# Optimization experiments

Hardware: AMD Instinct MI355X
Metric: run time of the kernel (lower is better)

Reference implementation:

```python
import jax, jax.numpy as jnp
import numpy as np

B, S, H, G, W_LOC = 2, 4096, 12, 64, 513  # Longformer-base: window=2*256+1, 64 global slots


def setup_inputs() -> dict:
    key = jax.random.key(0)
    k1, = jax.random.split(key, 1)
    attention_probs = jax.random.uniform(k1, (B, S, H, G + W_LOC), dtype=jnp.float32)
    attention_mask = jnp.zeros((B, S), dtype=jnp.float32)  # all tokens currently kept
    # global tokens are the first G positions of every batch; nonzero(as_tuple) index arrays
    b_idx = jnp.repeat(jnp.arange(B, dtype=jnp.int64), G)
    g_idx = jnp.tile(jnp.arange(G, dtype=jnp.int64), B)
    return {
        "attention_mask": attention_mask,
        "attention_probs": attention_probs,
        "keep_threshold": jnp.asarray(0.005, dtype=jnp.float32),  # base 0.01*6/12 + learned 0
        "max_num_global_attn_indices": G,
        "loc_b": b_idx, "loc_i": g_idx,
        "glob_b": b_idx, "glob_i": g_idx,
    }


def reference(attention_mask, attention_probs, keep_threshold,
              max_num_global_attn_indices, loc_b, loc_i, glob_b, glob_i):
    Gn = max_num_global_attn_indices
    b, s, h, wg = attention_probs.shape
    w = wg - Gn  # local window size, odd
    half = w // 2

    # zero out rows of already-masked tokens (attention_mask < 0)
    probs = jnp.where((attention_mask < 0)[:, :, None, None], 0.0, attention_probs)

    gl = probs[..., :Gn]                              # [B,S,H,G]
    lo = jnp.transpose(probs[..., Gn:], (0, 2, 1, 3))  # [B,H,S,W]

    # anti-diagonal (key-column) sums of the local band; equals the source's
    # conv2d-with-flipped-identity + slice: out[j] = sum_c lo[j + half - c, c]
    lo_p = jnp.pad(lo, ((0, 0), (0, 0), (half, half), (0, 0)))  # [B,H,S+W-1,W]
    rows = jnp.arange(s)[:, None] + (w - 1) - jnp.arange(w)[None, :]  # [S,W]
    diag = lo_p[:, :, rows, jnp.arange(w)[None, :]]  # [B,H,S,W]
    local_sum = diag.sum(axis=(1, 3))                # [B,S] (summed over heads too)

    global_sum = gl.sum(axis=(1, 2))                 # [B,G]
    probs_sum = local_sum.at[loc_b, loc_i].add(global_sum[glob_b, glob_i])

    probs_max = probs_sum.max(axis=-1, keepdims=True)
    scores = probs_sum / probs_max

    thr = jnp.maximum(jnp.float32(1e-5), jnp.asarray(keep_threshold, jnp.float32).reshape(()))
    new_attention_mask = jnp.where(scores < thr, jnp.float32(-10000.0), jnp.float32(0.0))
    return new_attention_mask, scores
```

## Files before the change

### kernel.cpp

```cpp
#include <hip/hip_runtime.h>
#include <float.h>

#define Bsz 2
#define Ssz 4096
#define Hsz 12
#define Gsz 64
#define Wsz 513
#define Csz (Gsz + Wsz)
#define ROW (Hsz * Csz)
#define HALF 256
#define RPB 16
#define WIN (RPB + Wsz - 1)

#define PSUM_SZ ((size_t)Bsz * Ssz)
#define GACC_SZ ((size_t)Bsz * Gsz)

__global__ __launch_bounds__(256) void k1_fused(
    const float* __restrict__ probs, const float* __restrict__ mask,
    float* __restrict__ psum, float* __restrict__ gacc)
{
    __shared__ float win[WIN];
    const int t = threadIdx.x;
    const int row0 = blockIdx.x * RPB;
    const int b = row0 / Ssz;
    float g = 0.f;

    for (int w = t; w < WIN; w += 256) win[w] = 0.f;
    __syncthreads();

    for (int r = 0; r < RPB; ++r) {
        const int row = row0 + r;
        const float* base = probs + (size_t)row * ROW;
        const float scale = (mask[row] < 0.f) ? 0.f : 1.f;

        float v0 = 0.f, v1 = 0.f, v2 = 0.f;
        #pragma unroll
        for (int h = 0; h < Hsz; ++h) {
            const float* hp = base + h * Csz;
            v0 += hp[t];
            v1 += hp[t + 256];
            if (t < Csz - 512)
                v2 += hp[t + 512];
        }
        v0 *= scale; v1 *= scale; v2 *= scale;

        if (t < Gsz) g += v0;
        else atomicAdd(&win[(t - Gsz) + r], v0);
        atomicAdd(&win[(t + 256 - Gsz) + r], v1);
        if (t < Csz - 512)
            atomicAdd(&win[(t + 512 - Gsz) + r], v2);
    }
    __syncthreads();

    const int i_base = (row0 - b * Ssz) - HALF;
    for (int w = t; w < WIN; w += 256) {
        const int i = i_base + w;
        if (i >= 0 && i < Ssz) atomicAdd(&psum[b * Ssz + i], win[w]);
    }
    if (t < Gsz) atomicAdd(&gacc[b * Gsz + t], g);
}

__global__ __launch_bounds__(1024) void k4_final(
    const float* __restrict__ psum, const float* __restrict__ thr_p,
    const int* __restrict__ loc_b, const int* __restrict__ loc_i,
    const int* __restrict__ glob_b, const int* __restrict__ glob_i,
    const float* __restrict__ gacc, int n_idx,
    float* __restrict__ out)
{
    const int b = blockIdx.x;
    const int t = threadIdx.x;
    __shared__ float sp[Ssz];
    const float* p = psum + (size_t)b * Ssz;

    for (int i = t; i < Ssz; i += 1024) sp[i] = p[i];
    __syncthreads();

    for (int k = t; k < n_idx; k += 1024)
        if (loc_b[k] == b)
            atomicAdd(&sp[loc_i[k]], gacc[glob_b[k] * Gsz + glob_i[k]]);
    __syncthreads();

    float m = -FLT_MAX;
    for (int i = t; i < Ssz; i += 1024) m = fmaxf(m, sp[i]);
    #pragma unroll
    for (int off = 32; off >= 1; off >>= 1) m = fmaxf(m, __shfl_down(m, off, 64));

    __shared__ float red[16];
    const int wave = t >> 6, lane = t & 63;
    if (lane == 0) red[wave] = m;
    __syncthreads();
    if (t == 0) {
        float mm = red[0];
        #pragma unroll
        for (int w = 1; w < 16; ++w) mm = fmaxf(mm, red[w]);
        red[0] = mm;
    }
    __syncthreads();
    const float mx = red[0];
    const float thr = fmaxf(1e-5f, thr_p[0]);

    for (int i = t; i < Ssz; i += 1024) {
        float sc = sp[i] / mx;
        out[(size_t)Bsz * Ssz + (size_t)b * Ssz + i] = sc;
        out[(size_t)b * Ssz + i] = (sc < thr) ? -10000.f : 0.f;
    }
}

extern "C" void kernel_launch(void* const* d_in, const int* in_sizes, int n_in,
                              void* d_out, int out_size, void* d_ws, size_t ws_size,
                              hipStream_t stream)
{
    const float* mask  = (const float*)d_in[0];
    const float* probs = (const float*)d_in[1];
    const float* thr   = (const float*)d_in[2];
    const int* loc_b  = (const int*)d_in[4];
    const int* loc_i  = (const int*)d_in[5];
    const int* glob_b = (const int*)d_in[6];
    const int* glob_i = (const int*)d_in[7];
    const int n_idx = in_sizes[4];

    float* psum = (float*)d_ws;
    float* gacc = psum + PSUM_SZ;
    float* out  = (float*)d_out;

    hipMemsetAsync(psum, 0, (PSUM_SZ + GACC_SZ) * sizeof(float), stream);

    k1_fused<<<dim3(Bsz * Ssz / RPB), dim3(256), 0, stream>>>(probs, mask, psum, gacc);
    k4_final<<<dim3(Bsz), dim3(1024), 0, stream>>>(psum, thr, loc_b, loc_i,
                                                   glob_b, glob_i, gacc, n_idx, out);
}
```

Baseline: 394.3 us.

## Load rows as float4 and scatter per element into swizzled shared window

The first kernel now reads each token row as 16-byte vector loads across all heads at once. Every element is then atomically added into a shared-memory window or a shared global-slot accumulator, where before each thread summed over heads in registers and issued one atomic. The window index is swizzled to spread LDS bank conflicts, and rows per block drop from 16 to 8 to give twice as many blocks. The aim is fully coalesced wide loads, at the cost of about twelve times more LDS atomics per row and more global atomics on psum.

```diff
diff --git a/kernel.cpp b/kernel.cpp
--- a/kernel.cpp
+++ b/kernel.cpp
@@ -8,56 +8,83 @@
 #define Wsz 513
 #define Csz (Gsz + Wsz)
 #define ROW (Hsz * Csz)
+#define QPR (ROW / 4)
 #define HALF 256
-#define RPB 16
+#define RPB 8
 #define WIN (RPB + Wsz - 1)
+#define WINP 544
 
 #define PSUM_SZ ((size_t)Bsz * Ssz)
 #define GACC_SZ ((size_t)Bsz * Gsz)
+
+__device__ __forceinline__ int swz(int x) {
+    return (x & ~31) | ((x + (x >> 5)) & 31);
+}
+
+__device__ __forceinline__ void scatter1(float v, int c, int r,
+                                         float* __restrict__ win,
+                                         float* __restrict__ gcc) {
+    if (c < Gsz) atomicAdd(&gcc[c], v);
+    else        atomicAdd(&win[swz(c - Gsz + r)], v);
+}
 
 __global__ __launch_bounds__(256) void k1_fused(
     const float* __restrict__ probs, const float* __restrict__ mask,
     float* __restrict__ psum, float* __restrict__ gacc)
 {
-    __shared__ float win[WIN];
+    __shared__ float win[WINP];
+    __shared__ float gcc[Gsz];
     const int t = threadIdx.x;
     const int row0 = blockIdx.x * RPB;
     const int b = row0 / Ssz;
-    float g = 0.f;
 
-    for (int w = t; w < WIN; w += 256) win[w] = 0.f;
+    for (int w = t; w < WINP; w += 256) win[w] = 0.f;
+    if (t < Gsz) gcc[t] = 0.f;
     __syncthreads();
+
+    int cb[7];
+    #pragma unroll
+    for (int k = 0; k < 7; ++k) cb[k] = (4 * (t + 256 * k)) % Csz;
+    const bool has7 = (t < QPR - 6 * 256);
 
     for (int r = 0; r < RPB; ++r) {
         const int row = row0 + r;
-        const float* base = probs + (size_t)row * ROW;
+        const float4* __restrict__ src = (const float4*)(probs + (size_t)row * ROW);
         const float scale = (mask[row] < 0.f) ? 0.f : 1.f;
 
-        float v0 = 0.f, v1 = 0.f, v2 = 0.f;
-        #pragma unroll
-        for (int h = 0; h < Hsz; ++h) {
-            const float* hp = base + h * Csz;
-            v0 += hp[t];
-            v1 += hp[t + 256];
-            if (t < Csz - 512)
-                v2 += hp[t + 512];
-        }
-        v0 *= scale; v1 *= scale; v2 *= scale;
+        float4 q0 = src[t];
+        float4 q1 = src[t + 256];
+        float4 q2 = src[t + 512];
+        float4 q3 = src[t + 768];
+        float4 q4 = src[t + 1024];
+        float4 q5 = src[t + 1280];
+        float4 q6 = make_float4(0.f, 0.f, 0.f, 0.f);
+        if (has7) q6 = src[t + 1536];
 
-        if (t < Gsz) g += v0;
-        else atomicAdd(&win[(t - Gsz) + r], v0);
-        atomicAdd(&win[(t + 256 - Gsz) + r], v1);
-        if (t < Csz - 512)
-            atomicAdd(&win[(t + 512 - Gsz) + r], v2);
+        #define PROC(Q, K) do {                                            \
+            int c0 = cb[K];                                                \
+            int c1 = c0 + 1; if (c1 >= Csz) c1 -= Csz;                     \
+            int c2 = c0 + 2; if (c2 >= Csz) c2 -= Csz;                     \
+            int c3 = c0 + 3; if (c3 >= Csz) c3 -= Csz;                     \
+            scatter1(Q.x * scale, c0, r, win, gcc);                        \
+            scatter1(Q.y * scale, c1, r, win, gcc);                        \
+            scatter1(Q.z * scale, c2, r, win, gcc);                        \
+            scatter1(Q.w * scale, c3, r, win, gcc);                        \
+        } while (0)
+
+        PROC(q0, 0); PROC(q1, 1); PROC(q2, 2);
+        PROC(q3, 3); PROC(q4, 4); PROC(q5, 5);
+        if (has7) PROC(q6, 6);
+        #undef PROC
     }
     __syncthreads();
 
     const int i_base = (row0 - b * Ssz) - HALF;
     for (int w = t; w < WIN; w += 256) {
         const int i = i_base + w;
-        if (i >= 0 && i < Ssz) atomicAdd(&psum[b * Ssz + i], win[w]);
+        if (i >= 0 && i < Ssz) atomicAdd(&psum[b * Ssz + i], win[swz(w)]);
     }
-    if (t < Gsz) atomicAdd(&gacc[b * Gsz + t], g);
+    if (t < Gsz) atomicAdd(&gacc[b * Gsz + t], gcc[t]);
 }
 
 __global__ __launch_bounds__(1024) void k4_final(
```

Result: slower. 524.7 us (+33.1%).
